# Kernel tuning notes

Hardware: AMD Instinct MI355X
Metric: run time of the kernel (lower is better)

## Reference

```python
import jax, jax.numpy as jnp
import numpy as np

EPS = 1e-3  # keras LayerNormalization default epsilon


def layer_norm(x, gamma, beta):
    mean = jnp.mean(x, axis=-1, keepdims=True)
    var = jnp.var(x, axis=-1, keepdims=True)
    return (x - mean) * jax.lax.rsqrt(var + EPS) * gamma + beta


def setup_inputs() -> dict:
    key = jax.random.key(0)
    ks = jax.random.split(key, 4)
    B, H, W, C, Ci = 16, 64, 64, 512, 64
    return {
        "x": jax.random.normal(ks[0], (B, H, W, C), dtype=jnp.float32),
        "Wf": jax.random.normal(ks[1], (C, Ci), dtype=jnp.float32) * (1.0 / np.sqrt(C)),
        "Wh": jax.random.normal(ks[2], (C, Ci), dtype=jnp.float32) * (1.0 / np.sqrt(C)),
        "Wfgh": jax.random.normal(ks[3], (Ci, C), dtype=jnp.float32) * (1.0 / np.sqrt(Ci)),
        "gamma_f": jnp.ones((Ci,), jnp.float32),
        "beta_f": jnp.zeros((Ci,), jnp.float32),
        "gamma_h": jnp.ones((Ci,), jnp.float32),
        "beta_h": jnp.zeros((Ci,), jnp.float32),
        "gamma_fgh": jnp.ones((C,), jnp.float32),
        "beta_fgh": jnp.zeros((C,), jnp.float32),
        "scale": jnp.ones((1,), jnp.float32),
    }


def reference(x, Wf, Wh, Wfgh, gamma_f, beta_f, gamma_h, beta_h, gamma_fgh, beta_fgh, scale):
    # NOTE: original code uses w_f / LN_f for BOTH f and g branches (w_g unused).
    fg_base = layer_norm(jnp.einsum("bhwc,cd->bhwd", x, Wf), gamma_f, beta_f)  # [B,H,W,Ci]
    f = jnp.transpose(fg_base, (0, 2, 1, 3))  # Permute(2,1,3): swap H and W
    g = fg_base
    h = layer_norm(jnp.einsum("bhwc,cd->bhwd", x, Wh), gamma_h, beta_h)
    attn = jax.nn.softmax(f * g, axis=1)  # softmax over height axis
    out = jnp.einsum("bhwd,dc->bhwc", attn * h, Wfgh)
    out = layer_norm(out, gamma_fgh, beta_fgh)
    return out * scale + x
```

## Files before the change

### kernel.cpp

```cpp
#include <hip/hip_runtime.h>
#include <math.h>

#define BB 16
#define HH 64
#define WW 64
#define CC 512
#define CI 64
#define NROWS (BB * HH * WW)
#define LN_EPS 1e-3f

typedef __attribute__((ext_vector_type(8))) short bf16x8;
typedef __attribute__((ext_vector_type(4))) float f32x4;

__device__ __forceinline__ unsigned short f2bf(float f) {
  union {
    float f;
    unsigned int u;
  } v;
  v.f = f;
  unsigned int r = v.u + 0x7FFF + ((v.u >> 16) & 1);
  return (unsigned short)(r >> 16);
}

__device__ __forceinline__ float bf2f(unsigned short u) {
  union {
    unsigned int u;
    float f;
  } v;
  v.u = ((unsigned int)u) << 16;
  return v.f;
}

__global__ __launch_bounds__(256) void sgsa_prep(
    const float* __restrict__ Wf, const float* __restrict__ Wh,
    const float* __restrict__ Wo, unsigned short* __restrict__ WcT,
    unsigned short* __restrict__ WoT) {
  int tid = blockIdx.x * 256 + threadIdx.x;
  for (int i = tid; i < 128 * 512; i += gridDim.x * 256) {
    int col = i >> 9, k = i & 511;
    float v = (col < 64) ? Wf[k * 64 + col] : Wh[k * 64 + (col - 64)];
    WcT[i] = f2bf(v);
  }
  for (int i = tid; i < 512 * 64; i += gridDim.x * 256) {
    int col = i >> 6, k = i & 63;
    WoT[i] = f2bf(Wo[k * 512 + col]);
  }
}

__global__ __launch_bounds__(256) void sgsa_k1_mfma(
    const float* __restrict__ x, const unsigned short* __restrict__ WcT,
    const float* __restrict__ gf, const float* __restrict__ bf,
    const float* __restrict__ gh, const float* __restrict__ bh,
    float* __restrict__ fg, float* __restrict__ hl) {
  const int lane = threadIdx.x & 63;
  const int wid = blockIdx.x * 4 + (threadIdx.x >> 6);
  const int row0 = wid * 32;
  const int cq = lane & 15;
  const int kg = lane >> 4;

  f32x4 acc[2][8];
#pragma unroll
  for (int rt = 0; rt < 2; ++rt)
#pragma unroll
    for (int ct = 0; ct < 8; ++ct) acc[rt][ct] = (f32x4){0.f, 0.f, 0.f, 0.f};

#pragma unroll 2
  for (int kk = 0; kk < 16; ++kk) {
    const int kb = kk * 32 + kg * 8;
    bf16x8 bfr[8];
#pragma unroll
    for (int ct = 0; ct < 8; ++ct) {
      const int col = ct * 16 + cq;
      bfr[ct] = *(const bf16x8*)&WcT[col * 512 + kb];
    }
#pragma unroll
    for (int rt = 0; rt < 2; ++rt) {
      const float* ap = &x[(size_t)(row0 + rt * 16 + cq) * CC + kb];
      f32x4 a0 = *(const f32x4*)ap;
      f32x4 a1 = *(const f32x4*)(ap + 4);
      bf16x8 af;
#pragma unroll
      for (int j = 0; j < 4; ++j) {
        af[j] = (short)f2bf(a0[j]);
        af[j + 4] = (short)f2bf(a1[j]);
      }
#pragma unroll
      for (int ct = 0; ct < 8; ++ct)
        acc[rt][ct] = __builtin_amdgcn_mfma_f32_16x16x32_bf16(
            af, bfr[ct], acc[rt][ct], 0, 0, 0);
    }
  }

  float gfv[4], bfv[4], ghv[4], bhv[4];
#pragma unroll
  for (int ct = 0; ct < 4; ++ct) {
    gfv[ct] = gf[ct * 16 + cq];
    bfv[ct] = bf[ct * 16 + cq];
    ghv[ct] = gh[ct * 16 + cq];
    bhv[ct] = bh[ct * 16 + cq];
  }

#pragma unroll
  for (int rt = 0; rt < 2; ++rt) {
#pragma unroll
    for (int r = 0; r < 4; ++r) {
      const int row = row0 + rt * 16 + kg * 4 + r;
      float s = acc[rt][0][r] + acc[rt][1][r] + acc[rt][2][r] + acc[rt][3][r];
      float q = acc[rt][0][r] * acc[rt][0][r] + acc[rt][1][r] * acc[rt][1][r] +
                acc[rt][2][r] * acc[rt][2][r] + acc[rt][3][r] * acc[rt][3][r];
#pragma unroll
      for (int m = 1; m < 16; m <<= 1) {
        s += __shfl_xor(s, m, 64);
        q += __shfl_xor(q, m, 64);
      }
      float mean = s * (1.f / 64.f);
      float var = q * (1.f / 64.f) - mean * mean;
      float inv = rsqrtf(var + LN_EPS);
#pragma unroll
      for (int ct = 0; ct < 4; ++ct) {
        float v = (acc[rt][ct][r] - mean) * inv * gfv[ct] + bfv[ct];
        fg[(size_t)row * CI + ct * 16 + cq] = v;
      }
      float s2 = acc[rt][4][r] + acc[rt][5][r] + acc[rt][6][r] + acc[rt][7][r];
      float q2 = acc[rt][4][r] * acc[rt][4][r] + acc[rt][5][r] * acc[rt][5][r] +
                 acc[rt][6][r] * acc[rt][6][r] + acc[rt][7][r] * acc[rt][7][r];
#pragma unroll
      for (int m = 1; m < 16; m <<= 1) {
        s2 += __shfl_xor(s2, m, 64);
        q2 += __shfl_xor(q2, m, 64);
      }
      float mean2 = s2 * (1.f / 64.f);
      float var2 = q2 * (1.f / 64.f) - mean2 * mean2;
      float inv2 = rsqrtf(var2 + LN_EPS);
#pragma unroll
      for (int ct = 0; ct < 4; ++ct) {
        float v = (acc[rt][ct + 4][r] - mean2) * inv2 * ghv[ct] + bhv[ct];
        hl[(size_t)row * CI + ct * 16 + cq] = v;
      }
    }
  }
}

__global__ __launch_bounds__(256) void sgsa_k23(
    const float* __restrict__ fg, const float* __restrict__ hl,
    const unsigned short* __restrict__ WoT, const float* __restrict__ go,
    const float* __restrict__ bo, const float* __restrict__ scale,
    const float* __restrict__ x, float* __restrict__ out) {
  const int b = blockIdx.x >> 6;
  const int w = blockIdx.x & 63;
  const int tid = threadIdx.x;

  __shared__ unsigned short t_hi[64 * 72];
  __shared__ unsigned short t_lo[64 * 72];
  __shared__ float red[4][64];
  __shared__ float s_red[4][64];
  __shared__ float q_red[4][64];

  {
    const int d = tid & 63;
    const int q = tid >> 6;
    const size_t base_g = (size_t)((b * 64) * 64 + w) * 64;
    const size_t base_f = (size_t)((b * 64 + w) * 64) * 64;

    float sv[16], hv[16];
#pragma unroll
    for (int i = 0; i < 16; ++i) {
      int h = q * 16 + i;
      float g = fg[base_g + (size_t)h * 4096 + d];
      float f = fg[base_f + (size_t)h * 64 + d];
      sv[i] = f * g;
      hv[i] = hl[base_g + (size_t)h * 4096 + d];
    }

    float m = sv[0];
#pragma unroll
    for (int i = 1; i < 16; ++i) m = fmaxf(m, sv[i]);
    red[q][d] = m;
    __syncthreads();
    m = fmaxf(fmaxf(red[0][d], red[1][d]), fmaxf(red[2][d], red[3][d]));
    __syncthreads();

    float ssum = 0.f;
#pragma unroll
    for (int i = 0; i < 16; ++i) {
      sv[i] = __expf(sv[i] - m);
      ssum += sv[i];
    }
    red[q][d] = ssum;
    __syncthreads();
    ssum = (red[0][d] + red[1][d]) + (red[2][d] + red[3][d]);
    float rinv = 1.f / ssum;

#pragma unroll
    for (int i = 0; i < 16; ++i) {
      int h = q * 16 + i;
      float t = sv[i] * rinv * hv[i];
      unsigned short th = f2bf(t);
      t_hi[h * 72 + d] = th;
      t_lo[h * 72 + d] = f2bf(t - bf2f(th));
    }
  }
  __syncthreads();

  const int lane = tid & 63;
  const int wv = tid >> 6;
  const int col0 = wv * 128;
  const int cq = lane & 15;
  const int kg = lane >> 4;

  f32x4 acc[4][8];
#pragma unroll
  for (int rt = 0; rt < 4; ++rt)
#pragma unroll
    for (int ct = 0; ct < 8; ++ct) acc[rt][ct] = (f32x4){0.f, 0.f, 0.f, 0.f};

#pragma unroll
  for (int kk = 0; kk < 2; ++kk) {
    const int kb = kk * 32 + kg * 8;
    bf16x8 bfr[8];
#pragma unroll
    for (int ct = 0; ct < 8; ++ct) {
      const int col = col0 + ct * 16 + cq;
      bfr[ct] = *(const bf16x8*)&WoT[col * CI + kb];
    }
#pragma unroll
    for (int rt = 0; rt < 4; ++rt) {
      bf16x8 ah = *(const bf16x8*)&t_hi[(rt * 16 + cq) * 72 + kb];
      bf16x8 al = *(const bf16x8*)&t_lo[(rt * 16 + cq) * 72 + kb];
#pragma unroll
      for (int ct = 0; ct < 8; ++ct) {
        acc[rt][ct] = __builtin_amdgcn_mfma_f32_16x16x32_bf16(
            ah, bfr[ct], acc[rt][ct], 0, 0, 0);
        acc[rt][ct] = __builtin_amdgcn_mfma_f32_16x16x32_bf16(
            al, bfr[ct], acc[rt][ct], 0, 0, 0);
      }
    }
  }

#pragma unroll
  for (int rt = 0; rt < 4; ++rt) {
#pragma unroll
    for (int r = 0; r < 4; ++r) {
      float s = 0.f, qq = 0.f;
#pragma unroll
      for (int ct = 0; ct < 8; ++ct) {
        float v = acc[rt][ct][r];
        s += v;
        qq += v * v;
      }
#pragma unroll
      for (int m = 1; m < 16; m <<= 1) {
        s += __shfl_xor(s, m, 64);
        qq += __shfl_xor(qq, m, 64);
      }
      if (cq == 0) {
        s_red[wv][rt * 16 + kg * 4 + r] = s;
        q_red[wv][rt * 16 + kg * 4 + r] = qq;
      }
    }
  }
  __syncthreads();

  const float sc = scale[0];
  float gov[8], bov[8];
#pragma unroll
  for (int ct = 0; ct < 8; ++ct) {
    gov[ct] = go[col0 + ct * 16 + cq];
    bov[ct] = bo[col0 + ct * 16 + cq];
  }

#pragma unroll
  for (int rt = 0; rt < 4; ++rt) {
#pragma unroll
    for (int r = 0; r < 4; ++r) {
      const int h = rt * 16 + kg * 4 + r;
      float s = (s_red[0][h] + s_red[1][h]) + (s_red[2][h] + s_red[3][h]);
      float q = (q_red[0][h] + q_red[1][h]) + (q_red[2][h] + q_red[3][h]);
      float mean = s * (1.f / 512.f);
      float var = q * (1.f / 512.f) - mean * mean;
      float inv = rsqrtf(var + LN_EPS);
      const size_t base = (size_t)((b * 64 + h) * 64 + w) * CC;
#pragma unroll
      for (int ct = 0; ct < 8; ++ct) {
        const int col = col0 + ct * 16 + cq;
        float o = (acc[rt][ct][r] - mean) * inv * gov[ct] + bov[ct];
        out[base + col] = o * sc + x[base + col];
      }
    }
  }
}

extern "C" void kernel_launch(void* const* d_in, const int* in_sizes, int n_in,
                              void* d_out, int out_size, void* d_ws,
                              size_t ws_size, hipStream_t stream) {
  const float* x = (const float*)d_in[0];
  const float* Wf = (const float*)d_in[1];
  const float* Wh = (const float*)d_in[2];
  const float* Wo = (const float*)d_in[3];
  const float* gf = (const float*)d_in[4];
  const float* bf = (const float*)d_in[5];
  const float* gh = (const float*)d_in[6];
  const float* bh = (const float*)d_in[7];
  const float* go = (const float*)d_in[8];
  const float* bo = (const float*)d_in[9];
  const float* sc = (const float*)d_in[10];
  float* out = (float*)d_out;

  unsigned short* WcT = (unsigned short*)d_ws;
  unsigned short* WoT = WcT + 128 * 512;
  float* fg = (float*)((char*)d_ws + (256 << 10));
  float* hl = fg + (size_t)NROWS * CI;

  sgsa_prep<<<128, 256, 0, stream>>>(Wf, Wh, Wo, WcT, WoT);
  sgsa_k1_mfma<<<NROWS / 128, 256, 0, stream>>>(x, WcT, gf, bf, gh, bh, fg,
                                                hl);
  sgsa_k23<<<BB * WW, 256, 0, stream>>>(fg, hl, WoT, go, bo, sc, x, out);
}
```

Measured before the change: 136.5 us.

## Shrink per-wave tiles and double k23 block size to raise occupancy

The projection kernel now gives each wave 16 rows instead of 32, doubling the grid. It also converts fp32 to bf16 with the packed v_cvt_pk_bf16_f32 instruction instead of manual rounding. The attention/output kernel moves to 512-thread blocks, splitting the 64 rows across two wave halves, and drops one barrier from the softmax reduction. Together these cut register pressure and raise occupancy, with launch_bounds hints added. The cost is more reloads of the weight fragments, since each wave now reuses them over fewer rows.

Result: slower. 159.0 us (+16.5%).

```diff
diff --git a/kernel.cpp b/kernel.cpp
--- a/kernel.cpp
+++ b/kernel.cpp
@@ -29,6 +29,12 @@
   } v;
   v.u = ((unsigned int)u) << 16;
   return v.f;
+}
+
+__device__ __forceinline__ unsigned int cvt_pk_bf16(float a, float b) {
+  unsigned int r;
+  asm("v_cvt_pk_bf16_f32 %0, %1, %2" : "=v"(r) : "v"(a), "v"(b));
+  return r;
 }
 
 __global__ __launch_bounds__(256) void sgsa_prep(
@@ -47,48 +53,44 @@
   }
 }
 
-__global__ __launch_bounds__(256) void sgsa_k1_mfma(
+__global__ __launch_bounds__(256, 4) void sgsa_k1_mfma(
     const float* __restrict__ x, const unsigned short* __restrict__ WcT,
     const float* __restrict__ gf, const float* __restrict__ bf,
     const float* __restrict__ gh, const float* __restrict__ bh,
     float* __restrict__ fg, float* __restrict__ hl) {
   const int lane = threadIdx.x & 63;
   const int wid = blockIdx.x * 4 + (threadIdx.x >> 6);
-  const int row0 = wid * 32;
+  const int row0 = wid * 16;
   const int cq = lane & 15;
   const int kg = lane >> 4;
 
-  f32x4 acc[2][8];
-#pragma unroll
-  for (int rt = 0; rt < 2; ++rt)
-#pragma unroll
-    for (int ct = 0; ct < 8; ++ct) acc[rt][ct] = (f32x4){0.f, 0.f, 0.f, 0.f};
+  f32x4 acc[8];
+#pragma unroll
+  for (int ct = 0; ct < 8; ++ct) acc[ct] = (f32x4){0.f, 0.f, 0.f, 0.f};
+
+  const float* __restrict__ arow = &x[(size_t)(row0 + cq) * CC];
 
 #pragma unroll 2
   for (int kk = 0; kk < 16; ++kk) {
     const int kb = kk * 32 + kg * 8;
     bf16x8 bfr[8];
 #pragma unroll
-    for (int ct = 0; ct < 8; ++ct) {
-      const int col = ct * 16 + cq;
-      bfr[ct] = *(const bf16x8*)&WcT[col * 512 + kb];
-    }
-#pragma unroll
-    for (int rt = 0; rt < 2; ++rt) {
-      const float* ap = &x[(size_t)(row0 + rt * 16 + cq) * CC + kb];
-      f32x4 a0 = *(const f32x4*)ap;
-      f32x4 a1 = *(const f32x4*)(ap + 4);
-      bf16x8 af;
-#pragma unroll
-      for (int j = 0; j < 4; ++j) {
-        af[j] = (short)f2bf(a0[j]);
-        af[j + 4] = (short)f2bf(a1[j]);
-      }
-#pragma unroll
-      for (int ct = 0; ct < 8; ++ct)
-        acc[rt][ct] = __builtin_amdgcn_mfma_f32_16x16x32_bf16(
-            af, bfr[ct], acc[rt][ct], 0, 0, 0);
-    }
+    for (int ct = 0; ct < 8; ++ct)
+      bfr[ct] = *(const bf16x8*)&WcT[(ct * 16 + cq) * 512 + kb];
+    f32x4 a0 = *(const f32x4*)(arow + kb);
+    f32x4 a1 = *(const f32x4*)(arow + kb + 4);
+    union {
+      bf16x8 v;
+      unsigned int u[4];
+    } af;
+    af.u[0] = cvt_pk_bf16(a0[0], a0[1]);
+    af.u[1] = cvt_pk_bf16(a0[2], a0[3]);
+    af.u[2] = cvt_pk_bf16(a1[0], a1[1]);
+    af.u[3] = cvt_pk_bf16(a1[2], a1[3]);
+#pragma unroll
+    for (int ct = 0; ct < 8; ++ct)
+      acc[ct] =
+          __builtin_amdgcn_mfma_f32_16x16x32_bf16(af.v, bfr[ct], acc[ct], 0, 0, 0);
   }
 
   float gfv[4], bfv[4], ghv[4], bhv[4];
@@ -101,47 +103,44 @@
   }
 
 #pragma unroll
-  for (int rt = 0; rt < 2; ++rt) {
-#pragma unroll
-    for (int r = 0; r < 4; ++r) {
-      const int row = row0 + rt * 16 + kg * 4 + r;
-      float s = acc[rt][0][r] + acc[rt][1][r] + acc[rt][2][r] + acc[rt][3][r];
-      float q = acc[rt][0][r] * acc[rt][0][r] + acc[rt][1][r] * acc[rt][1][r] +
-                acc[rt][2][r] * acc[rt][2][r] + acc[rt][3][r] * acc[rt][3][r];
-#pragma unroll
-      for (int m = 1; m < 16; m <<= 1) {
-        s += __shfl_xor(s, m, 64);
-        q += __shfl_xor(q, m, 64);
-      }
-      float mean = s * (1.f / 64.f);
-      float var = q * (1.f / 64.f) - mean * mean;
-      float inv = rsqrtf(var + LN_EPS);
-#pragma unroll
-      for (int ct = 0; ct < 4; ++ct) {
-        float v = (acc[rt][ct][r] - mean) * inv * gfv[ct] + bfv[ct];
-        fg[(size_t)row * CI + ct * 16 + cq] = v;
-      }
-      float s2 = acc[rt][4][r] + acc[rt][5][r] + acc[rt][6][r] + acc[rt][7][r];
-      float q2 = acc[rt][4][r] * acc[rt][4][r] + acc[rt][5][r] * acc[rt][5][r] +
-                 acc[rt][6][r] * acc[rt][6][r] + acc[rt][7][r] * acc[rt][7][r];
-#pragma unroll
-      for (int m = 1; m < 16; m <<= 1) {
-        s2 += __shfl_xor(s2, m, 64);
-        q2 += __shfl_xor(q2, m, 64);
-      }
-      float mean2 = s2 * (1.f / 64.f);
-      float var2 = q2 * (1.f / 64.f) - mean2 * mean2;
-      float inv2 = rsqrtf(var2 + LN_EPS);
-#pragma unroll
-      for (int ct = 0; ct < 4; ++ct) {
-        float v = (acc[rt][ct + 4][r] - mean2) * inv2 * ghv[ct] + bhv[ct];
-        hl[(size_t)row * CI + ct * 16 + cq] = v;
-      }
-    }
-  }
-}
-
-__global__ __launch_bounds__(256) void sgsa_k23(
+  for (int r = 0; r < 4; ++r) {
+    const int row = row0 + kg * 4 + r;
+    float s = acc[0][r] + acc[1][r] + acc[2][r] + acc[3][r];
+    float q = acc[0][r] * acc[0][r] + acc[1][r] * acc[1][r] +
+              acc[2][r] * acc[2][r] + acc[3][r] * acc[3][r];
+#pragma unroll
+    for (int m = 1; m < 16; m <<= 1) {
+      s += __shfl_xor(s, m, 64);
+      q += __shfl_xor(q, m, 64);
+    }
+    float mean = s * (1.f / 64.f);
+    float var = q * (1.f / 64.f) - mean * mean;
+    float inv = rsqrtf(var + LN_EPS);
+#pragma unroll
+    for (int ct = 0; ct < 4; ++ct) {
+      float v = (acc[ct][r] - mean) * inv * gfv[ct] + bfv[ct];
+      fg[(size_t)row * CI + ct * 16 + cq] = v;
+    }
+    float s2 = acc[4][r] + acc[5][r] + acc[6][r] + acc[7][r];
+    float q2 = acc[4][r] * acc[4][r] + acc[5][r] * acc[5][r] +
+               acc[6][r] * acc[6][r] + acc[7][r] * acc[7][r];
+#pragma unroll
+    for (int m = 1; m < 16; m <<= 1) {
+      s2 += __shfl_xor(s2, m, 64);
+      q2 += __shfl_xor(q2, m, 64);
+    }
+    float mean2 = s2 * (1.f / 64.f);
+    float var2 = q2 * (1.f / 64.f) - mean2 * mean2;
+    float inv2 = rsqrtf(var2 + LN_EPS);
+#pragma unroll
+    for (int ct = 0; ct < 4; ++ct) {
+      float v = (acc[ct + 4][r] - mean2) * inv2 * ghv[ct] + bhv[ct];
+      hl[(size_t)row * CI + ct * 16 + cq] = v;
+    }
+  }
+}
+
+__global__ __launch_bounds__(512, 4) void sgsa_k23(
     const float* __restrict__ fg, const float* __restrict__ hl,
     const unsigned short* __restrict__ WoT, const float* __restrict__ go,
     const float* __restrict__ bo, const float* __restrict__ scale,
@@ -152,20 +151,21 @@
 
   __shared__ unsigned short t_hi[64 * 72];
   __shared__ unsigned short t_lo[64 * 72];
-  __shared__ float red[4][64];
-  __shared__ float s_red[4][64];
-  __shared__ float q_red[4][64];
+  __shared__ float redA[8][64];
+  __shared__ float redB[8][64];
+  __shared__ float s_red[8][32];
+  __shared__ float q_red[8][32];
 
   {
     const int d = tid & 63;
     const int q = tid >> 6;
-    const size_t base_g = (size_t)((b * 64) * 64 + w) * 64;
-    const size_t base_f = (size_t)((b * 64 + w) * 64) * 64;
-
-    float sv[16], hv[16];
-#pragma unroll
-    for (int i = 0; i < 16; ++i) {
-      int h = q * 16 + i;
+    const size_t base_g = ((size_t)(b * 64) * 64 + w) * 64;
+    const size_t base_f = ((size_t)(b * 64 + w) * 64) * 64;
+
+    float sv[8], hv[8];
+#pragma unroll
+    for (int i = 0; i < 8; ++i) {
+      int h = q * 8 + i;
       float g = fg[base_g + (size_t)h * 4096 + d];
       float f = fg[base_f + (size_t)h * 64 + d];
       sv[i] = f * g;
@@ -174,26 +174,28 @@
 
     float m = sv[0];
 #pragma unroll
-    for (int i = 1; i < 16; ++i) m = fmaxf(m, sv[i]);
-    red[q][d] = m;
+    for (int i = 1; i < 8; ++i) m = fmaxf(m, sv[i]);
+    redA[q][d] = m;
     __syncthreads();
-    m = fmaxf(fmaxf(red[0][d], red[1][d]), fmaxf(red[2][d], red[3][d]));
-    __syncthreads();
+#pragma unroll
+    for (int j = 0; j < 8; ++j) m = fmaxf(m, redA[j][d]);
 
     float ssum = 0.f;
 #pragma unroll
-    for (int i = 0; i < 16; ++i) {
+    for (int i = 0; i < 8; ++i) {
       sv[i] = __expf(sv[i] - m);
       ssum += sv[i];
     }
-    red[q][d] = ssum;
+    redB[q][d] = ssum;
     __syncthreads();
-    ssum = (red[0][d] + red[1][d]) + (red[2][d] + red[3][d]);
+    ssum = 0.f;
+#pragma unroll
+    for (int j = 0; j < 8; ++j) ssum += redB[j][d];
     float rinv = 1.f / ssum;
 
 #pragma unroll
-    for (int i = 0; i < 16; ++i) {
-      int h = q * 16 + i;
+    for (int i = 0; i < 8; ++i) {
+      int h = q * 8 + i;
       float t = sv[i] * rinv * hv[i];
       unsigned short th = f2bf(t);
       t_hi[h * 72 + d] = th;
@@ -204,41 +206,52 @@
 
   const int lane = tid & 63;
   const int wv = tid >> 6;
-  const int col0 = wv * 128;
+  const int rh = wv >> 2;
+  const int cw = wv & 3;
+  const int col0 = cw * 128;
   const int cq = lane & 15;
   const int kg = lane >> 4;
-
-  f32x4 acc[4][8];
-#pragma unroll
-  for (int rt = 0; rt < 4; ++rt)
+  const int trow0 = rh * 32;
+
+  f32x4 acc[2][8];
+#pragma unroll
+  for (int rt = 0; rt < 2; ++rt)
 #pragma unroll
     for (int ct = 0; ct < 8; ++ct) acc[rt][ct] = (f32x4){0.f, 0.f, 0.f, 0.f};
 
 #pragma unroll
   for (int kk = 0; kk < 2; ++kk) {
     const int kb = kk * 32 + kg * 8;
-    bf16x8 bfr[8];
-#pragma unroll
-    for (int ct = 0; ct < 8; ++ct) {
-      const int col = col0 + ct * 16 + cq;
-      bfr[ct] = *(const bf16x8*)&WoT[col * CI + kb];
-    }
-#pragma unroll
-    for (int rt = 0; rt < 4; ++rt) {
-      bf16x8 ah = *(const bf16x8*)&t_hi[(rt * 16 + cq) * 72 + kb];
-      bf16x8 al = *(const bf16x8*)&t_lo[(rt * 16 + cq) * 72 + kb];
-#pragma unroll
-      for (int ct = 0; ct < 8; ++ct) {
-        acc[rt][ct] = __builtin_amdgcn_mfma_f32_16x16x32_bf16(
-            ah, bfr[ct], acc[rt][ct], 0, 0, 0);
-        acc[rt][ct] = __builtin_amdgcn_mfma_f32_16x16x32_bf16(
-            al, bfr[ct], acc[rt][ct], 0, 0, 0);
-      }
-    }
-  }
-
-#pragma unroll
-  for (int rt = 0; rt < 4; ++rt) {
+    bf16x8 ah[2], al[2];
+#pragma unroll
+    for (int rt = 0; rt < 2; ++rt) {
+      ah[rt] = *(const bf16x8*)&t_hi[(trow0 + rt * 16 + cq) * 72 + kb];
+      al[rt] = *(const bf16x8*)&t_lo[(trow0 + rt * 16 + cq) * 72 + kb];
+    }
+#pragma unroll
+    for (int half = 0; half < 2; ++half) {
+      bf16x8 bfr[4];
+#pragma unroll
+      for (int c4 = 0; c4 < 4; ++c4) {
+        const int ct = half * 4 + c4;
+        bfr[c4] = *(const bf16x8*)&WoT[(col0 + ct * 16 + cq) * CI + kb];
+      }
+#pragma unroll
+      for (int rt = 0; rt < 2; ++rt) {
+#pragma unroll
+        for (int c4 = 0; c4 < 4; ++c4) {
+          const int ct = half * 4 + c4;
+          acc[rt][ct] = __builtin_amdgcn_mfma_f32_16x16x32_bf16(
+              ah[rt], bfr[c4], acc[rt][ct], 0, 0, 0);
+          acc[rt][ct] = __builtin_amdgcn_mfma_f32_16x16x32_bf16(
+              al[rt], bfr[c4], acc[rt][ct], 0, 0, 0);
+        }
+      }
+    }
+  }
+
+#pragma unroll
+  for (int rt = 0; rt < 2; ++rt) {
 #pragma unroll
     for (int r = 0; r < 4; ++r) {
       float s = 0.f, qq = 0.f;
@@ -270,12 +283,15 @@
   }
 
 #pragma unroll
-  for (int rt = 0; rt < 4; ++rt) {
+  for (int rt = 0; rt < 2; ++rt) {
 #pragma unroll
     for (int r = 0; r < 4; ++r) {
-      const int h = rt * 16 + kg * 4 + r;
-      float s = (s_red[0][h] + s_red[1][h]) + (s_red[2][h] + s_red[3][h]);
-      float q = (q_red[0][h] + q_red[1][h]) + (q_red[2][h] + q_red[3][h]);
+      const int rl = rt * 16 + kg * 4 + r;
+      const int h = trow0 + rl;
+      float s = (s_red[rh * 4 + 0][rl] + s_red[rh * 4 + 1][rl]) +
+                (s_red[rh * 4 + 2][rl] + s_red[rh * 4 + 3][rl]);
+      float q = (q_red[rh * 4 + 0][rl] + q_red[rh * 4 + 1][rl]) +
+                (q_red[rh * 4 + 2][rl] + q_red[rh * 4 + 3][rl]);
       float mean = s * (1.f / 512.f);
       float var = q * (1.f / 512.f) - mean * mean;
       float inv = rsqrtf(var + LN_EPS);
@@ -312,7 +328,6 @@
   float* hl = fg + (size_t)NROWS * CI;
 
   sgsa_prep<<<128, 256, 0, stream>>>(Wf, Wh, Wo, WcT, WoT);
-  sgsa_k1_mfma<<<NROWS / 128, 256, 0, stream>>>(x, WcT, gf, bf, gh, bh, fg,
-                                                hl);
-  sgsa_k23<<<BB * WW, 256, 0, stream>>>(fg, hl, WoT, go, bo, sc, x, out);
-}
+  sgsa_k1_mfma<<<NROWS / 64, 256, 0, stream>>>(x, WcT, gf, bf, gh, bh, fg, hl);
+  sgsa_k23<<<BB * WW, 512, 0, stream>>>(fg, hl, WoT, go, bo, sc, x, out);
+}
```
